# Kernel optimization log

Measured on AMD Instinct MI355X. Metric: run time of the kernel, lower is better.

Reference implementation:

```python
import jax, jax.numpy as jnp
import numpy as np

PROCESS_INIT = 1.0
OBSERVATION_INIT = 1.0


def _build_dynamics_A(K, fut_len):
    # shift-structured single-modal A: state slot i takes value of slot i+1, last step repeats
    sd = 2 * fut_len
    a = np.zeros((sd, sd), dtype=np.float32)
    for i in range(fut_len - 1):
        a[2 * i, 2 * i + 2] = 1.0
        a[2 * i + 1, 2 * i + 3] = 1.0
    a[sd - 2, sd - 2] = 1.0
    a[sd - 1, sd - 1] = 1.0
    # block-diagonal over K modes
    return jnp.asarray(np.kron(np.eye(K, dtype=np.float32), a))


def setup_inputs() -> dict:
    key = jax.random.key(0)
    ks = jax.random.split(key, 6)
    B, A, K, fut_len = 2, 32, 6, 30
    D = K * 2 * fut_len  # 360
    belief_mean = jax.random.normal(ks[0], (B, A, D), dtype=jnp.float32)
    M = jax.random.normal(ks[1], (B, A, D, D), dtype=jnp.float32)
    # symmetric, SPD (eigenvalues ~ 2 +/- 0.2) so linear solves are well-posed
    belief_covariance = 0.003 * (M + jnp.swapaxes(M, -1, -2)) + 2.0 * jnp.eye(D, dtype=jnp.float32)
    observations = jax.random.normal(ks[2], (B, A, D), dtype=jnp.float32)
    rs = jax.random.uniform(ks[3], (B, A), dtype=jnp.float32)
    initialized = jax.random.bernoulli(ks[4], 0.7, (B, A))
    selected = jax.random.bernoulli(ks[5], 0.8, (B, A))
    return {
        "belief_mean": belief_mean,
        "belief_covariance": belief_covariance,
        "observations": observations,
        "rs": rs,
        "initialized": initialized,
        "selected": selected,
        "K": K,
        "fut_len": fut_len,
    }


def reference(belief_mean, belief_covariance, observations, rs, initialized, selected, K, fut_len):
    D = K * 2 * fut_len
    A = _build_dynamics_A(K, fut_len)  # [D, D], static sparse shift structure
    I = jnp.eye(D, dtype=belief_mean.dtype)
    r_obs = (rs + OBSERVATION_INIT)[..., None, None]  # [B, A, 1, 1]

    init_new = selected & (~initialized)  # first observation of agent
    upd = selected & initialized          # predict + Kalman update

    # --- initialization branch ---
    mean_init = observations
    cov_init = belief_covariance + r_obs * I

    # --- predict step: m <- A m ; P <- A P A^T + Q, Q = process_init * I ---
    m_pred = belief_mean @ A.T  # [B, A, D]
    P_pred = jnp.einsum('ij,bnjk,lk->bnil', A, belief_covariance, A) + PROCESS_INIT * I

    # --- update step (H = I): S = P + R ; Kg = P S^{-1} ---
    S = P_pred + r_obs * I
    Kg = P_pred @ jnp.linalg.inv(S)
    m_upd = m_pred + jnp.einsum('bnij,bnj->bni', Kg, observations - m_pred)
    P_upd = (I - Kg) @ P_pred

    # --- scatter the three branches back (masked merge) ---
    mean_out = jnp.where(init_new[..., None], mean_init,
               jnp.where(upd[..., None], m_upd, belief_mean))
    cov_out = jnp.where(init_new[..., None, None], cov_init,
              jnp.where(upd[..., None, None], P_upd, belief_covariance))
    initialized_out = initialized | selected
    return mean_out, cov_out, initialized_out
```

## Files before the change

kernel.cpp:

```cpp
#include <hip/hip_runtime.h>

#define D 360
#define NAG 64
#define NB 60
#define NPAN 6
#define COV_OFF (NAG * D)
#define INIT_OFF (COV_OFF + NAG * D * D)
#define RBOFF(par, ag, ct) ((((par) * NAG + (ag)) * 6 + (ct)) * 3600)

__device__ __forceinline__ int gshift(int i) {
    return ((i % 60) < 58) ? (i + 2) : i;
}

__global__ __launch_bounds__(384) void build_kernel(
    const float* __restrict__ P, const float* __restrict__ mean_in,
    const float* __restrict__ obs, const float* __restrict__ rs,
    const int* __restrict__ init_f, const int* __restrict__ sel_f,
    float* __restrict__ out, float* __restrict__ rb)
{
    const int by = blockIdx.x, ag = blockIdx.y, t = threadIdx.x;
    const bool ini = init_f[ag] != 0, sel = sel_f[ag] != 0;
    const float c = rs[ag] + 1.0f;
    if (by == 45) {
        if (t < D) {
            float v = (sel && !ini) ? obs[ag * D + t] : mean_in[ag * D + t];
            out[ag * D + t] = v;
        }
        if (t == 0) out[INIT_OFF + ag] = (ini || sel) ? 1.0f : 0.0f;
        return;
    }
    if (t >= D) return;
    const float* Pa = P + (size_t)ag * D * D;
    float* cov = out + COV_OFF + (size_t)ag * D * D;
    const int j = t;
    if (sel && ini) {
        const int gj = gshift(j);
        #pragma unroll
        for (int s = 0; s < 8; ++s) {
            const int i = by * 8 + s;
            float v = Pa[(size_t)gshift(i) * D + gj];
            if (i == j) v += 1.0f + c;
            cov[(size_t)i * D + j] = v;
            if (i < NB && j >= NB)
                rb[RBOFF(0, ag, j / NB) + i * NB + (j % NB)] = v;
        }
    } else if (sel) {
        #pragma unroll
        for (int s = 0; s < 8; ++s) {
            const int i = by * 8 + s;
            cov[(size_t)i * D + j] = Pa[(size_t)i * D + j] + ((i == j) ? c : 0.0f);
        }
    } else {
        #pragma unroll
        for (int s = 0; s < 8; ++s) {
            const int i = by * 8 + s;
            cov[(size_t)i * D + j] = Pa[(size_t)i * D + j];
        }
    }
}

__device__ __forceinline__ void inv4(float4& m0, float4& m1, float4& m2, float4& m3)
{
    float pv, f;
    pv = 1.0f / m0.x;
    m0.y *= pv; m0.z *= pv; m0.w *= pv; m0.x = pv;
    f = m1.x; m1.y = fmaf(-f, m0.y, m1.y); m1.z = fmaf(-f, m0.z, m1.z); m1.w = fmaf(-f, m0.w, m1.w); m1.x = -f * pv;
    f = m2.x; m2.y = fmaf(-f, m0.y, m2.y); m2.z = fmaf(-f, m0.z, m2.z); m2.w = fmaf(-f, m0.w, m2.w); m2.x = -f * pv;
    f = m3.x; m3.y = fmaf(-f, m0.y, m3.y); m3.z = fmaf(-f, m0.z, m3.z); m3.w = fmaf(-f, m0.w, m3.w); m3.x = -f * pv;
    pv = 1.0f / m1.y;
    m1.x *= pv; m1.z *= pv; m1.w *= pv; m1.y = pv;
    f = m0.y; m0.x = fmaf(-f, m1.x, m0.x); m0.z = fmaf(-f, m1.z, m0.z); m0.w = fmaf(-f, m1.w, m0.w); m0.y = -f * pv;
    f = m2.y; m2.x = fmaf(-f, m1.x, m2.x); m2.z = fmaf(-f, m1.z, m2.z); m2.w = fmaf(-f, m1.w, m2.w); m2.y = -f * pv;
    f = m3.y; m3.x = fmaf(-f, m1.x, m3.x); m3.z = fmaf(-f, m1.z, m3.z); m3.w = fmaf(-f, m1.w, m3.w); m3.y = -f * pv;
    pv = 1.0f / m2.z;
    m2.x *= pv; m2.y *= pv; m2.w *= pv; m2.z = pv;
    f = m0.z; m0.x = fmaf(-f, m2.x, m0.x); m0.y = fmaf(-f, m2.y, m0.y); m0.w = fmaf(-f, m2.w, m0.w); m0.z = -f * pv;
    f = m1.z; m1.x = fmaf(-f, m2.x, m1.x); m1.y = fmaf(-f, m2.y, m1.y); m1.w = fmaf(-f, m2.w, m1.w); m1.z = -f * pv;
    f = m3.z; m3.x = fmaf(-f, m2.x, m3.x); m3.y = fmaf(-f, m2.y, m3.y); m3.w = fmaf(-f, m2.w, m3.w); m3.z = -f * pv;
    pv = 1.0f / m3.w;
    m3.x *= pv; m3.y *= pv; m3.z *= pv; m3.w = pv;
    f = m0.w; m0.x = fmaf(-f, m3.x, m0.x); m0.y = fmaf(-f, m3.y, m0.y); m0.z = fmaf(-f, m3.z, m0.z); m0.w = -f * pv;
    f = m1.w; m1.x = fmaf(-f, m3.x, m1.x); m1.y = fmaf(-f, m3.y, m1.y); m1.z = fmaf(-f, m3.z, m1.z); m1.w = -f * pv;
    f = m2.w; m2.x = fmaf(-f, m3.x, m2.x); m2.y = fmaf(-f, m3.y, m2.y); m2.z = fmaf(-f, m3.z, m2.z); m2.w = -f * pv;
}

__global__ __launch_bounds__(384) void factor_kernel(
    float* __restrict__ out, const int* __restrict__ init_f,
    const int* __restrict__ sel_f, float* __restrict__ rb, int p)
{
    const int ag = blockIdx.x;
    if (!(init_f[ag] && sel_f[ag])) return;
    float* M = out + COV_OFF + (size_t)ag * D * D;
    const int j0 = p * NB;
    const int r = threadIdx.x;
    const int rel = r - j0;
    float4 row[15];
    if (r < D) {
        const float* src = M + (size_t)r * D + j0;
        #pragma unroll
        for (int q = 0; q < 15; ++q) row[q] = *(const float4*)(src + 4 * q);
    }
    __shared__ float4 praw[2][4][15];
    if (rel >= 0 && rel < 4) {
        #pragma unroll
        for (int q = 0; q < 15; ++q) praw[0][rel][q] = row[q];
    }
    __syncthreads();
    #pragma unroll
    for (int kb = 0; kb < 15; ++kb) {
        const int buf = kb & 1;
        float4 m0 = praw[buf][0][kb];
        float4 m1 = praw[buf][1][kb];
        float4 m2 = praw[buf][2][kb];
        float4 m3 = praw[buf][3][kb];
        inv4(m0, m1, m2, m3);
        if (r < D) {
            const bool is_piv = (rel >= 4 * kb) && (rel < 4 * kb + 4);
            float4 sc;
            if (is_piv) {
                const int i = rel - 4 * kb;
                sc = (i == 0) ? m0 : (i == 1) ? m1 : (i == 2) ? m2 : m3;
                #pragma unroll
                for (int q = 0; q < 15; ++q)
                    if (q != kb) row[q] = make_float4(0.f, 0.f, 0.f, 0.f);
            } else {
                float4 fr = row[kb];
                sc.x = -(fr.x * m0.x + fr.y * m1.x + fr.z * m2.x + fr.w * m3.x);
                sc.y = -(fr.x * m0.y + fr.y * m1.y + fr.z * m2.y + fr.w * m3.y);
                sc.z = -(fr.x * m0.z + fr.y * m1.z + fr.z * m2.z + fr.w * m3.z);
                sc.w = -(fr.x * m0.w + fr.y * m1.w + fr.z * m2.w + fr.w * m3.w);
            }
            #pragma unroll
            for (int q = 0; q < 15; ++q) {
                if (q == kb) continue;
                float4 p0 = praw[buf][0][q];
                float4 p1 = praw[buf][1][q];
                float4 p2 = praw[buf][2][q];
                float4 p3 = praw[buf][3][q];
                row[q].x = fmaf(sc.x, p0.x, fmaf(sc.y, p1.x, fmaf(sc.z, p2.x, fmaf(sc.w, p3.x, row[q].x))));
                row[q].y = fmaf(sc.x, p0.y, fmaf(sc.y, p1.y, fmaf(sc.z, p2.y, fmaf(sc.w, p3.y, row[q].y))));
                row[q].z = fmaf(sc.x, p0.z, fmaf(sc.y, p1.z, fmaf(sc.z, p2.z, fmaf(sc.w, p3.z, row[q].z))));
                row[q].w = fmaf(sc.x, p0.w, fmaf(sc.y, p1.w, fmaf(sc.z, p2.w, fmaf(sc.w, p3.w, row[q].w))));
            }
            row[kb] = sc;
            if (kb < 14 && rel >= 4 * (kb + 1) && rel < 4 * (kb + 1) + 4) {
                const int i = rel - 4 * (kb + 1);
                #pragma unroll
                for (int q = 0; q < 15; ++q) praw[buf ^ 1][i][q] = row[q];
            }
        }
        __syncthreads();
    }
    if (r < D) {
        float* dst = M + (size_t)r * D + j0;
        #pragma unroll
        for (int q = 0; q < 15; ++q) *(float4*)(dst + 4 * q) = row[q];
        if (p < NPAN - 1) {
            const int nrel = r - NB * (p + 1);
            if (nrel >= 0 && nrel < NB) {
                float* rdst = rb + RBOFF((p + 1) & 1, ag, p) + nrel * NB;
                #pragma unroll
                for (int q = 0; q < 15; ++q) *(float4*)(rdst + 4 * q) = row[q];
            }
        }
    }
}

__device__ __forceinline__ void mm_row(const float4 a, const float4 b0, const float4 b1,
                                       const float4 b2, const float4 b3, float acc[4]) {
    acc[0] = fmaf(a.x, b0.x, fmaf(a.y, b1.x, fmaf(a.z, b2.x, fmaf(a.w, b3.x, acc[0]))));
    acc[1] = fmaf(a.x, b0.y, fmaf(a.y, b1.y, fmaf(a.z, b2.y, fmaf(a.w, b3.y, acc[1]))));
    acc[2] = fmaf(a.x, b0.z, fmaf(a.y, b1.z, fmaf(a.z, b2.z, fmaf(a.w, b3.z, acc[2]))));
    acc[3] = fmaf(a.x, b0.w, fmaf(a.y, b1.w, fmaf(a.z, b2.w, fmaf(a.w, b3.w, acc[3]))));
}

__global__ __launch_bounds__(256) void update_kernel(
    float* __restrict__ out, const float* __restrict__ rs,
    const int* __restrict__ init_f, const int* __restrict__ sel_f,
    float* __restrict__ rb, int p)
{
    const int ag = blockIdx.x;
    if (!(init_f[ag] && sel_f[ag])) return;
    const int ct = blockIdx.y + (blockIdx.y >= p ? 1 : 0);
    float* M = out + COV_OFF + (size_t)ag * D * D;
    const int j0 = p * NB, c0 = ct * NB;
    const float c = rs[ag] + 1.0f;
    const float c2 = c * c;
    __shared__ float R[NB][NB + 8];
    __shared__ float F[NB][NB + 8];
    const int t = threadIdx.x;
    {
        const float* rsrc = rb + RBOFF(p & 1, ag, ct);
        for (int idx = t; idx < NB * 15; idx += 256) {
            int k = idx / 15, q = idx % 15;
            *(float4*)&R[k][4 * q] = *(const float4*)(rsrc + k * NB + 4 * q);
        }
    }
    const int tx = t % 16, ty = t / 16;
    for (int rr = 0; rr < 2; ++rr) {
        const int rt = (int)blockIdx.z * 2 + rr;
        const int r0 = rt * NB;
        __syncthreads();
        for (int idx = t; idx < NB * 15; idx += 256) {
            int rrw = idx / 15, q = idx % 15;
            *(float4*)&F[rrw][4 * q] = *(const float4*)(M + (size_t)(r0 + rrw) * D + j0 + 4 * q);
        }
        __syncthreads();
        if (tx < 15 && ty < 15) {
            float acc[4][4];
            #pragma unroll
            for (int i = 0; i < 4; ++i)
                #pragma unroll
                for (int j = 0; j < 4; ++j) acc[i][j] = 0.0f;
            for (int kq = 0; kq < 15; ++kq) {
                float4 a0 = *(const float4*)&F[4 * ty + 0][4 * kq];
                float4 a1 = *(const float4*)&F[4 * ty + 1][4 * kq];
                float4 a2 = *(const float4*)&F[4 * ty + 2][4 * kq];
                float4 a3 = *(const float4*)&F[4 * ty + 3][4 * kq];
                float4 b0 = *(const float4*)&R[4 * kq + 0][4 * tx];
                float4 b1 = *(const float4*)&R[4 * kq + 1][4 * tx];
                float4 b2 = *(const float4*)&R[4 * kq + 2][4 * tx];
                float4 b3 = *(const float4*)&R[4 * kq + 3][4 * tx];
                mm_row(a0, b0, b1, b2, b3, acc[0]);
                mm_row(a1, b0, b1, b2, b3, acc[1]);
                mm_row(a2, b0, b1, b2, b3, acc[2]);
                mm_row(a3, b0, b1, b2, b3, acc[3]);
            }
            #pragma unroll
            for (int i = 0; i < 4; ++i) {
                const int rg = r0 + 4 * ty + i;
                float* dst = M + (size_t)rg * D + c0 + 4 * tx;
                float4 base;
                if (rt == p) { base = make_float4(0.f, 0.f, 0.f, 0.f); }
                else         { base = *(const float4*)dst; }
                float4 v;
                v.x = base.x + acc[i][0];
                v.y = base.y + acc[i][1];
                v.z = base.z + acc[i][2];
                v.w = base.w + acc[i][3];
                if (p < NPAN - 1) {
                    if (rt == p + 1 && ct != p + 1) {
                        float* rdst = rb + RBOFF((p + 1) & 1, ag, ct) + (4 * ty + i) * NB + 4 * tx;
                        *(float4*)rdst = v;
                    }
                    *(float4*)dst = v;
                } else {
                    const int cg = c0 + 4 * tx;
                    float4 o;
                    o.x = ((rg == cg + 0) ? c : 0.f) - c2 * v.x;
                    o.y = ((rg == cg + 1) ? c : 0.f) - c2 * v.y;
                    o.z = ((rg == cg + 2) ? c : 0.f) - c2 * v.z;
                    o.w = ((rg == cg + 3) ? c : 0.f) - c2 * v.w;
                    *(float4*)dst = o;
                }
            }
        }
    }
}

__global__ __launch_bounds__(384) void fin_panel_kernel(
    float* __restrict__ out, const float* __restrict__ rs,
    const int* __restrict__ init_f, const int* __restrict__ sel_f)
{
    const int ag = blockIdx.x;
    if (!(init_f[ag] && sel_f[ag])) return;
    const int t = threadIdx.x;
    if (t >= 360) return;
    const float c = rs[ag] + 1.0f;
    const float c2 = c * c;
    float* cov = out + COV_OFF + (size_t)ag * D * D;
    const int r = (int)blockIdx.y * 6 + t / 60;
    const int cc = (NPAN - 1) * NB + (t % 60);
    const float v = cov[(size_t)r * D + cc];
    cov[(size_t)r * D + cc] = ((r == cc) ? c : 0.f) - c2 * v;
}

__global__ __launch_bounds__(384) void solve_mean_kernel(
    float* __restrict__ out, const float* __restrict__ mean_in,
    const float* __restrict__ obs, const float* __restrict__ rs,
    const int* __restrict__ init_f, const int* __restrict__ sel_f)
{
    const int ag = blockIdx.x;
    if (!(init_f[ag] && sel_f[ag])) return;
    const float* C = out + COV_OFF + (size_t)ag * D * D;
    __shared__ float dsh[D];
    const int t = threadIdx.x;
    if (t < D) dsh[t] = obs[ag * D + t] - mean_in[ag * D + gshift(t)];
    __syncthreads();
    if (t < D) {
        float dot = 0.0f;
        #pragma unroll 8
        for (int j = 0; j < D; ++j)
            dot = fmaf(C[(size_t)j * D + t], dsh[j], dot);
        const float c = rs[ag] + 1.0f;
        out[ag * D + t] = obs[ag * D + t] - dsh[t] + dot / c;
    }
}

extern "C" void kernel_launch(void* const* d_in, const int* in_sizes, int n_in,
                              void* d_out, int out_size, void* d_ws, size_t ws_size,
                              hipStream_t stream) {
    const float* mean_in     = (const float*)d_in[0];
    const float* P           = (const float*)d_in[1];
    const float* obs         = (const float*)d_in[2];
    const float* rs          = (const float*)d_in[3];
    const int*   initialized = (const int*)d_in[4];
    const int*   selected    = (const int*)d_in[5];
    float* out = (float*)d_out;
    float* rb  = (float*)d_ws;

    build_kernel<<<dim3(46, NAG), 384, 0, stream>>>(P, mean_in, obs, rs,
                                                    initialized, selected, out, rb);
    for (int p = 0; p < NPAN; ++p) {
        factor_kernel<<<NAG, 384, 0, stream>>>(out, initialized, selected, rb, p);
        update_kernel<<<dim3(NAG, NPAN - 1, 3), 256, 0, stream>>>(out, rs, initialized,
                                                                  selected, rb, p);
    }
    fin_panel_kernel<<<dim3(NAG, 60), 384, 0, stream>>>(out, rs, initialized, selected);
    solve_mean_kernel<<<NAG, 384, 0, stream>>>(out, mean_in, obs, rs, initialized, selected);
}
```

Measured before the change: 312.9 us.

## Widen Gauss-Jordan panels to 120 columns and fold final panel scaling

Raises the block Gauss-Jordan inversion panel width from 60 to 120, so the factor/update loop runs 3 times instead of 6. That halves the kernel launches and the global round trips of the trailing matrix. The update kernel now handles 60x60 output tiles with a 120-deep inner product, and the factor kernel applies the final (c - c^2*X) transform for the last panel, which removes the separate fin_panel kernel. In exchange each factor thread holds 30 float4 registers and runs 30 serial 4x4 pivot steps, which may hurt occupancy and lengthen the serial factor phase.

```diff
diff --git a/kernel.cpp b/kernel.cpp
--- a/kernel.cpp
+++ b/kernel.cpp
@@ -2,11 +2,12 @@
 
 #define D 360
 #define NAG 64
-#define NB 60
-#define NPAN 6
+#define NB 120
+#define NPAN 3
+#define NQ 30
 #define COV_OFF (NAG * D)
 #define INIT_OFF (COV_OFF + NAG * D * D)
-#define RBOFF(par, ag, ct) ((((par) * NAG + (ag)) * 6 + (ct)) * 3600)
+#define SB(par, ag, slot) ((((size_t)(par) * NAG + (ag)) * 4 + (slot)) * 7200)
 
 __device__ __forceinline__ int gshift(int i) {
     return ((i % 60) < 58) ? (i + 2) : i;
@@ -42,7 +43,7 @@
             if (i == j) v += 1.0f + c;
             cov[(size_t)i * D + j] = v;
             if (i < NB && j >= NB)
-                rb[RBOFF(0, ag, j / NB) + i * NB + (j % NB)] = v;
+                rb[SB(0, ag, j / 60 - 2) + i * 60 + (j % 60)] = v;
         }
     } else if (sel) {
         #pragma unroll
@@ -84,9 +85,69 @@
     f = m2.w; m2.x = fmaf(-f, m3.x, m2.x); m2.y = fmaf(-f, m3.y, m2.y); m2.z = fmaf(-f, m3.z, m2.z); m2.w = -f * pv;
 }
 
+template<int KB>
+__device__ __forceinline__ void gj_step(float4 (&row)[NQ], int r, int rel,
+                                        float4 (&praw)[2][4][NQ])
+{
+    const int buf = KB & 1;
+    float4 m0 = praw[buf][0][KB];
+    float4 m1 = praw[buf][1][KB];
+    float4 m2 = praw[buf][2][KB];
+    float4 m3 = praw[buf][3][KB];
+    inv4(m0, m1, m2, m3);
+    if (r < D) {
+        const bool is_piv = (rel >= 4 * KB) && (rel < 4 * KB + 4);
+        float4 sc;
+        if (is_piv) {
+            const int i = rel - 4 * KB;
+            sc = (i == 0) ? m0 : (i == 1) ? m1 : (i == 2) ? m2 : m3;
+            #pragma unroll
+            for (int q = 0; q < NQ; ++q)
+                if (q != KB) row[q] = make_float4(0.f, 0.f, 0.f, 0.f);
+        } else {
+            float4 fr = row[KB];
+            sc.x = -(fr.x * m0.x + fr.y * m1.x + fr.z * m2.x + fr.w * m3.x);
+            sc.y = -(fr.x * m0.y + fr.y * m1.y + fr.z * m2.y + fr.w * m3.y);
+            sc.z = -(fr.x * m0.z + fr.y * m1.z + fr.z * m2.z + fr.w * m3.z);
+            sc.w = -(fr.x * m0.w + fr.y * m1.w + fr.z * m2.w + fr.w * m3.w);
+        }
+        #pragma unroll
+        for (int q = 0; q < NQ; ++q) {
+            if (q == KB) continue;
+            float4 p0 = praw[buf][0][q];
+            float4 p1 = praw[buf][1][q];
+            float4 p2 = praw[buf][2][q];
+            float4 p3 = praw[buf][3][q];
+            row[q].x = fmaf(sc.x, p0.x, fmaf(sc.y, p1.x, fmaf(sc.z, p2.x, fmaf(sc.w, p3.x, row[q].x))));
+            row[q].y = fmaf(sc.x, p0.y, fmaf(sc.y, p1.y, fmaf(sc.z, p2.y, fmaf(sc.w, p3.y, row[q].y))));
+            row[q].z = fmaf(sc.x, p0.z, fmaf(sc.y, p1.z, fmaf(sc.z, p2.z, fmaf(sc.w, p3.z, row[q].z))));
+            row[q].w = fmaf(sc.x, p0.w, fmaf(sc.y, p1.w, fmaf(sc.z, p2.w, fmaf(sc.w, p3.w, row[q].w))));
+        }
+        row[KB] = sc;
+        if (KB < NQ - 1 && rel >= 4 * (KB + 1) && rel < 4 * (KB + 1) + 4) {
+            const int i = rel - 4 * (KB + 1);
+            #pragma unroll
+            for (int q = 0; q < NQ; ++q) praw[buf ^ 1][i][q] = row[q];
+        }
+    }
+    __syncthreads();
+}
+
+template<int KB> struct GJSteps {
+    __device__ static __forceinline__ void run(float4 (&row)[NQ], int r, int rel,
+                                               float4 (&praw)[2][4][NQ]) {
+        gj_step<KB>(row, r, rel, praw);
+        GJSteps<KB + 1>::run(row, r, rel, praw);
+    }
+};
+template<> struct GJSteps<NQ> {
+    __device__ static __forceinline__ void run(float4 (&)[NQ], int, int, float4 (&)[2][4][NQ]) {}
+};
+
 __global__ __launch_bounds__(384) void factor_kernel(
-    float* __restrict__ out, const int* __restrict__ init_f,
-    const int* __restrict__ sel_f, float* __restrict__ rb, int p)
+    float* __restrict__ out, const float* __restrict__ rs,
+    const int* __restrict__ init_f, const int* __restrict__ sel_f,
+    float* __restrict__ rb, int p)
 {
     const int ag = blockIdx.x;
     if (!(init_f[ag] && sel_f[ag])) return;
@@ -94,73 +155,45 @@
     const int j0 = p * NB;
     const int r = threadIdx.x;
     const int rel = r - j0;
-    float4 row[15];
+    float4 row[NQ];
     if (r < D) {
         const float* src = M + (size_t)r * D + j0;
         #pragma unroll
-        for (int q = 0; q < 15; ++q) row[q] = *(const float4*)(src + 4 * q);
-    }
-    __shared__ float4 praw[2][4][15];
+        for (int q = 0; q < NQ; ++q) row[q] = *(const float4*)(src + 4 * q);
+    }
+    __shared__ float4 praw[2][4][NQ];
     if (rel >= 0 && rel < 4) {
         #pragma unroll
-        for (int q = 0; q < 15; ++q) praw[0][rel][q] = row[q];
+        for (int q = 0; q < NQ; ++q) praw[0][rel][q] = row[q];
     }
     __syncthreads();
-    #pragma unroll
-    for (int kb = 0; kb < 15; ++kb) {
-        const int buf = kb & 1;
-        float4 m0 = praw[buf][0][kb];
-        float4 m1 = praw[buf][1][kb];
-        float4 m2 = praw[buf][2][kb];
-        float4 m3 = praw[buf][3][kb];
-        inv4(m0, m1, m2, m3);
-        if (r < D) {
-            const bool is_piv = (rel >= 4 * kb) && (rel < 4 * kb + 4);
-            float4 sc;
-            if (is_piv) {
-                const int i = rel - 4 * kb;
-                sc = (i == 0) ? m0 : (i == 1) ? m1 : (i == 2) ? m2 : m3;
-                #pragma unroll
-                for (int q = 0; q < 15; ++q)
-                    if (q != kb) row[q] = make_float4(0.f, 0.f, 0.f, 0.f);
-            } else {
-                float4 fr = row[kb];
-                sc.x = -(fr.x * m0.x + fr.y * m1.x + fr.z * m2.x + fr.w * m3.x);
-                sc.y = -(fr.x * m0.y + fr.y * m1.y + fr.z * m2.y + fr.w * m3.y);
-                sc.z = -(fr.x * m0.z + fr.y * m1.z + fr.z * m2.z + fr.w * m3.z);
-                sc.w = -(fr.x * m0.w + fr.y * m1.w + fr.z * m2.w + fr.w * m3.w);
-            }
-            #pragma unroll
-            for (int q = 0; q < 15; ++q) {
-                if (q == kb) continue;
-                float4 p0 = praw[buf][0][q];
-                float4 p1 = praw[buf][1][q];
-                float4 p2 = praw[buf][2][q];
-                float4 p3 = praw[buf][3][q];
-                row[q].x = fmaf(sc.x, p0.x, fmaf(sc.y, p1.x, fmaf(sc.z, p2.x, fmaf(sc.w, p3.x, row[q].x))));
-                row[q].y = fmaf(sc.x, p0.y, fmaf(sc.y, p1.y, fmaf(sc.z, p2.y, fmaf(sc.w, p3.y, row[q].y))));
-                row[q].z = fmaf(sc.x, p0.z, fmaf(sc.y, p1.z, fmaf(sc.z, p2.z, fmaf(sc.w, p3.z, row[q].z))));
-                row[q].w = fmaf(sc.x, p0.w, fmaf(sc.y, p1.w, fmaf(sc.z, p2.w, fmaf(sc.w, p3.w, row[q].w))));
-            }
-            row[kb] = sc;
-            if (kb < 14 && rel >= 4 * (kb + 1) && rel < 4 * (kb + 1) + 4) {
-                const int i = rel - 4 * (kb + 1);
-                #pragma unroll
-                for (int q = 0; q < 15; ++q) praw[buf ^ 1][i][q] = row[q];
-            }
-        }
-        __syncthreads();
-    }
+    GJSteps<0>::run(row, r, rel, praw);
     if (r < D) {
         float* dst = M + (size_t)r * D + j0;
-        #pragma unroll
-        for (int q = 0; q < 15; ++q) *(float4*)(dst + 4 * q) = row[q];
-        if (p < NPAN - 1) {
+        if (p == NPAN - 1) {
+            const float c = rs[ag] + 1.0f;
+            const float c2 = c * c;
+            #pragma unroll
+            for (int q = 0; q < NQ; ++q) {
+                const int cg = j0 + 4 * q;
+                float4 o;
+                o.x = ((r == cg + 0) ? c : 0.f) - c2 * row[q].x;
+                o.y = ((r == cg + 1) ? c : 0.f) - c2 * row[q].y;
+                o.z = ((r == cg + 2) ? c : 0.f) - c2 * row[q].z;
+                o.w = ((r == cg + 3) ? c : 0.f) - c2 * row[q].w;
+                *(float4*)(dst + 4 * q) = o;
+            }
+        } else {
+            #pragma unroll
+            for (int q = 0; q < NQ; ++q) *(float4*)(dst + 4 * q) = row[q];
             const int nrel = r - NB * (p + 1);
             if (nrel >= 0 && nrel < NB) {
-                float* rdst = rb + RBOFF((p + 1) & 1, ag, p) + nrel * NB;
                 #pragma unroll
-                for (int q = 0; q < 15; ++q) *(float4*)(rdst + 4 * q) = row[q];
+                for (int q = 0; q < NQ; ++q) {
+                    const int slot = 2 * p + (q >= 15);
+                    float* rdst = rb + SB((p + 1) & 1, ag, slot) + nrel * 60 + (q % 15) * 4;
+                    *(float4*)rdst = row[q];
+                }
             }
         }
     }
@@ -181,98 +214,90 @@
 {
     const int ag = blockIdx.x;
     if (!(init_f[ag] && sel_f[ag])) return;
-    const int ct = blockIdx.y + (blockIdx.y >= p ? 1 : 0);
+    const int y = blockIdx.y;
+    const int ct = y + (y >= 2 * p ? 2 : 0);
+    const int rt = blockIdx.z;
+    const int r0 = 60 * rt, c0 = 60 * ct;
+    const bool panelrow = ((rt >> 1) == p);
     float* M = out + COV_OFF + (size_t)ag * D * D;
-    const int j0 = p * NB, c0 = ct * NB;
     const float c = rs[ag] + 1.0f;
     const float c2 = c * c;
-    __shared__ float R[NB][NB + 8];
-    __shared__ float F[NB][NB + 8];
+    __shared__ float R[NB][60];
+    __shared__ float F[60][NB + 4];
     const int t = threadIdx.x;
     {
-        const float* rsrc = rb + RBOFF(p & 1, ag, ct);
-        for (int idx = t; idx < NB * 15; idx += 256) {
-            int k = idx / 15, q = idx % 15;
-            *(float4*)&R[k][4 * q] = *(const float4*)(rsrc + k * NB + 4 * q);
-        }
-    }
+        const float* rsrc = rb + SB(p & 1, ag, y);
+        for (int idx = t; idx < 120 * 15; idx += 256) {
+            const int k = idx / 15, q = idx % 15;
+            *(float4*)&R[k][4 * q] = *(const float4*)(rsrc + k * 60 + 4 * q);
+        }
+    }
+    {
+        for (int idx = t; idx < 60 * NQ; idx += 256) {
+            const int row = idx / NQ, q = idx % NQ;
+            float4 v = *(const float4*)(M + (size_t)(r0 + row) * D + p * NB + 4 * q);
+            if (p == NPAN - 1) {
+                const int rg = r0 + row, cg = p * NB + 4 * q;
+                v.x = (((rg == cg + 0) ? c : 0.f) - v.x) / c2;
+                v.y = (((rg == cg + 1) ? c : 0.f) - v.y) / c2;
+                v.z = (((rg == cg + 2) ? c : 0.f) - v.z) / c2;
+                v.w = (((rg == cg + 3) ? c : 0.f) - v.w) / c2;
+            }
+            *(float4*)&F[row][4 * q] = v;
+        }
+    }
+    __syncthreads();
     const int tx = t % 16, ty = t / 16;
-    for (int rr = 0; rr < 2; ++rr) {
-        const int rt = (int)blockIdx.z * 2 + rr;
-        const int r0 = rt * NB;
-        __syncthreads();
-        for (int idx = t; idx < NB * 15; idx += 256) {
-            int rrw = idx / 15, q = idx % 15;
-            *(float4*)&F[rrw][4 * q] = *(const float4*)(M + (size_t)(r0 + rrw) * D + j0 + 4 * q);
-        }
-        __syncthreads();
-        if (tx < 15 && ty < 15) {
-            float acc[4][4];
-            #pragma unroll
-            for (int i = 0; i < 4; ++i)
-                #pragma unroll
-                for (int j = 0; j < 4; ++j) acc[i][j] = 0.0f;
-            for (int kq = 0; kq < 15; ++kq) {
-                float4 a0 = *(const float4*)&F[4 * ty + 0][4 * kq];
-                float4 a1 = *(const float4*)&F[4 * ty + 1][4 * kq];
-                float4 a2 = *(const float4*)&F[4 * ty + 2][4 * kq];
-                float4 a3 = *(const float4*)&F[4 * ty + 3][4 * kq];
-                float4 b0 = *(const float4*)&R[4 * kq + 0][4 * tx];
-                float4 b1 = *(const float4*)&R[4 * kq + 1][4 * tx];
-                float4 b2 = *(const float4*)&R[4 * kq + 2][4 * tx];
-                float4 b3 = *(const float4*)&R[4 * kq + 3][4 * tx];
-                mm_row(a0, b0, b1, b2, b3, acc[0]);
-                mm_row(a1, b0, b1, b2, b3, acc[1]);
-                mm_row(a2, b0, b1, b2, b3, acc[2]);
-                mm_row(a3, b0, b1, b2, b3, acc[3]);
+    if (tx < 15 && ty < 15) {
+        float acc[4][4];
+        #pragma unroll
+        for (int i = 0; i < 4; ++i)
+            #pragma unroll
+            for (int j = 0; j < 4; ++j) acc[i][j] = 0.0f;
+        for (int kq = 0; kq < NQ; ++kq) {
+            float4 a0 = *(const float4*)&F[4 * ty + 0][4 * kq];
+            float4 a1 = *(const float4*)&F[4 * ty + 1][4 * kq];
+            float4 a2 = *(const float4*)&F[4 * ty + 2][4 * kq];
+            float4 a3 = *(const float4*)&F[4 * ty + 3][4 * kq];
+            float4 b0 = *(const float4*)&R[4 * kq + 0][4 * tx];
+            float4 b1 = *(const float4*)&R[4 * kq + 1][4 * tx];
+            float4 b2 = *(const float4*)&R[4 * kq + 2][4 * tx];
+            float4 b3 = *(const float4*)&R[4 * kq + 3][4 * tx];
+            mm_row(a0, b0, b1, b2, b3, acc[0]);
+            mm_row(a1, b0, b1, b2, b3, acc[1]);
+            mm_row(a2, b0, b1, b2, b3, acc[2]);
+            mm_row(a3, b0, b1, b2, b3, acc[3]);
+        }
+        #pragma unroll
+        for (int i = 0; i < 4; ++i) {
+            const int rg = r0 + 4 * ty + i;
+            float* dst = M + (size_t)rg * D + c0 + 4 * tx;
+            float4 base;
+            if (panelrow) { base = make_float4(0.f, 0.f, 0.f, 0.f); }
+            else          { base = *(const float4*)dst; }
+            float4 v;
+            v.x = base.x + acc[i][0];
+            v.y = base.y + acc[i][1];
+            v.z = base.z + acc[i][2];
+            v.w = base.w + acc[i][3];
+            if (p < NPAN - 1) {
+                if ((rt >> 1) == p + 1 && (ct >> 1) != p + 1) {
+                    const int slot = ct - (ct > 2 * p + 3 ? 2 : 0);
+                    const int srow = rg - NB * (p + 1);
+                    *(float4*)(rb + SB((p + 1) & 1, ag, slot) + srow * 60 + 4 * tx) = v;
+                }
+                *(float4*)dst = v;
+            } else {
+                const int cg = c0 + 4 * tx;
+                float4 o;
+                o.x = ((rg == cg + 0) ? c : 0.f) - c2 * v.x;
+                o.y = ((rg == cg + 1) ? c : 0.f) - c2 * v.y;
+                o.z = ((rg == cg + 2) ? c : 0.f) - c2 * v.z;
+                o.w = ((rg == cg + 3) ? c : 0.f) - c2 * v.w;
+                *(float4*)dst = o;
             }
-            #pragma unroll
-            for (int i = 0; i < 4; ++i) {
-                const int rg = r0 + 4 * ty + i;
-                float* dst = M + (size_t)rg * D + c0 + 4 * tx;
-                float4 base;
-                if (rt == p) { base = make_float4(0.f, 0.f, 0.f, 0.f); }
-                else         { base = *(const float4*)dst; }
-                float4 v;
-                v.x = base.x + acc[i][0];
-                v.y = base.y + acc[i][1];
-                v.z = base.z + acc[i][2];
-                v.w = base.w + acc[i][3];
-                if (p < NPAN - 1) {
-                    if (rt == p + 1 && ct != p + 1) {
-                        float* rdst = rb + RBOFF((p + 1) & 1, ag, ct) + (4 * ty + i) * NB + 4 * tx;
-                        *(float4*)rdst = v;
-                    }
-                    *(float4*)dst = v;
-                } else {
-                    const int cg = c0 + 4 * tx;
-                    float4 o;
-                    o.x = ((rg == cg + 0) ? c : 0.f) - c2 * v.x;
-                    o.y = ((rg == cg + 1) ? c : 0.f) - c2 * v.y;
-                    o.z = ((rg == cg + 2) ? c : 0.f) - c2 * v.z;
-                    o.w = ((rg == cg + 3) ? c : 0.f) - c2 * v.w;
-                    *(float4*)dst = o;
-                }
-            }
-        }
-    }
-}
-
-__global__ __launch_bounds__(384) void fin_panel_kernel(
-    float* __restrict__ out, const float* __restrict__ rs,
-    const int* __restrict__ init_f, const int* __restrict__ sel_f)
-{
-    const int ag = blockIdx.x;
-    if (!(init_f[ag] && sel_f[ag])) return;
-    const int t = threadIdx.x;
-    if (t >= 360) return;
-    const float c = rs[ag] + 1.0f;
-    const float c2 = c * c;
-    float* cov = out + COV_OFF + (size_t)ag * D * D;
-    const int r = (int)blockIdx.y * 6 + t / 60;
-    const int cc = (NPAN - 1) * NB + (t % 60);
-    const float v = cov[(size_t)r * D + cc];
-    cov[(size_t)r * D + cc] = ((r == cc) ? c : 0.f) - c2 * v;
+        }
+    }
 }
 
 __global__ __launch_bounds__(384) void solve_mean_kernel(
@@ -312,10 +337,9 @@
     build_kernel<<<dim3(46, NAG), 384, 0, stream>>>(P, mean_in, obs, rs,
                                                     initialized, selected, out, rb);
     for (int p = 0; p < NPAN; ++p) {
-        factor_kernel<<<NAG, 384, 0, stream>>>(out, initialized, selected, rb, p);
-        update_kernel<<<dim3(NAG, NPAN - 1, 3), 256, 0, stream>>>(out, rs, initialized,
-                                                                  selected, rb, p);
-    }
-    fin_panel_kernel<<<dim3(NAG, 60), 384, 0, stream>>>(out, rs, initialized, selected);
+        factor_kernel<<<NAG, 384, 0, stream>>>(out, rs, initialized, selected, rb, p);
+        update_kernel<<<dim3(NAG, 4, 6), 256, 0, stream>>>(out, rs, initialized,
+                                                           selected, rb, p);
+    }
     solve_mean_kernel<<<NAG, 384, 0, stream>>>(out, mean_in, obs, rs, initialized, selected);
 }
```

New measurement: 366.1 us. +17.0%, slower.

## Stage factor panel in shared memory with 540 threads; fold final panel transform

Applied to the files above, without the earlier changes.

The panel factorization now keeps the 360x60 slab in shared memory and spreads it over 540 threads, each handling one float4 column chunk for ten rows. Before, each of 360 threads held a full 60-wide row in registers. The aim is more parallelism per block and lower register pressure in the serial per-panel step. The final-panel output transform is now applied inside factor_kernel for the last panel, and update_kernel undoes it when reading that panel. This removes the separate fin_panel_kernel launch, at the cost of extra LDS traffic and a divide in the update loads.

```diff
diff --git a/kernel.cpp b/kernel.cpp
--- a/kernel.cpp
+++ b/kernel.cpp
@@ -4,6 +4,7 @@
 #define NAG 64
 #define NB 60
 #define NPAN 6
+#define FTH 540
 #define COV_OFF (NAG * D)
 #define INIT_OFF (COV_OFF + NAG * D * D)
 #define RBOFF(par, ag, ct) ((((par) * NAG + (ag)) * 6 + (ct)) * 3600)
@@ -84,84 +85,96 @@
     f = m2.w; m2.x = fmaf(-f, m3.x, m2.x); m2.y = fmaf(-f, m3.y, m2.y); m2.z = fmaf(-f, m3.z, m2.z); m2.w = -f * pv;
 }
 
-__global__ __launch_bounds__(384) void factor_kernel(
-    float* __restrict__ out, const int* __restrict__ init_f,
-    const int* __restrict__ sel_f, float* __restrict__ rb, int p)
+__global__ __launch_bounds__(FTH) void factor_kernel(
+    float* __restrict__ out, const float* __restrict__ rs,
+    const int* __restrict__ init_f, const int* __restrict__ sel_f,
+    float* __restrict__ rb, int p)
 {
     const int ag = blockIdx.x;
     if (!(init_f[ag] && sel_f[ag])) return;
     float* M = out + COV_OFF + (size_t)ag * D * D;
     const int j0 = p * NB;
-    const int r = threadIdx.x;
-    const int rel = r - j0;
-    float4 row[15];
-    if (r < D) {
-        const float* src = M + (size_t)r * D + j0;
-        #pragma unroll
-        for (int q = 0; q < 15; ++q) row[q] = *(const float4*)(src + 4 * q);
-    }
+    const int t = threadIdx.x;
+    __shared__ float  slab[D][NB];
     __shared__ float4 praw[2][4][15];
-    if (rel >= 0 && rel < 4) {
-        #pragma unroll
-        for (int q = 0; q < 15; ++q) praw[0][rel][q] = row[q];
+    __shared__ float4 fcol[2][D];
+    const int q  = t % 15;
+    const int r0 = t / 15;
+    #pragma unroll
+    for (int k = 0; k < 10; ++k) {
+        const int r = r0 + 36 * k;
+        *(float4*)&slab[r][4 * q] = *(const float4*)(M + (size_t)r * D + j0 + 4 * q);
     }
     __syncthreads();
-    #pragma unroll
+    if (t < 60) praw[0][t / 15][t % 15] = *(float4*)&slab[j0 + t / 15][4 * (t % 15)];
+    if (t < D)  fcol[0][t] = *(float4*)&slab[t][0];
+    __syncthreads();
+
     for (int kb = 0; kb < 15; ++kb) {
         const int buf = kb & 1;
-        float4 m0 = praw[buf][0][kb];
-        float4 m1 = praw[buf][1][kb];
-        float4 m2 = praw[buf][2][kb];
-        float4 m3 = praw[buf][3][kb];
+        float4 m0 = praw[buf][0][kb], m1 = praw[buf][1][kb],
+               m2 = praw[buf][2][kb], m3 = praw[buf][3][kb];
         inv4(m0, m1, m2, m3);
-        if (r < D) {
-            const bool is_piv = (rel >= 4 * kb) && (rel < 4 * kb + 4);
+        const int pr0 = j0 + 4 * kb;
+        #pragma unroll
+        for (int k = 0; k < 10; ++k) {
+            const int r = r0 + 36 * k;
+            const int ii = r - pr0;
+            const bool ispiv = (ii >= 0) && (ii < 4);
             float4 sc;
-            if (is_piv) {
-                const int i = rel - 4 * kb;
-                sc = (i == 0) ? m0 : (i == 1) ? m1 : (i == 2) ? m2 : m3;
-                #pragma unroll
-                for (int q = 0; q < 15; ++q)
-                    if (q != kb) row[q] = make_float4(0.f, 0.f, 0.f, 0.f);
+            if (ispiv) {
+                sc = (ii == 0) ? m0 : (ii == 1) ? m1 : (ii == 2) ? m2 : m3;
             } else {
-                float4 fr = row[kb];
+                const float4 fr = fcol[buf][r];
                 sc.x = -(fr.x * m0.x + fr.y * m1.x + fr.z * m2.x + fr.w * m3.x);
                 sc.y = -(fr.x * m0.y + fr.y * m1.y + fr.z * m2.y + fr.w * m3.y);
                 sc.z = -(fr.x * m0.z + fr.y * m1.z + fr.z * m2.z + fr.w * m3.z);
                 sc.w = -(fr.x * m0.w + fr.y * m1.w + fr.z * m2.w + fr.w * m3.w);
             }
-            #pragma unroll
-            for (int q = 0; q < 15; ++q) {
-                if (q == kb) continue;
-                float4 p0 = praw[buf][0][q];
-                float4 p1 = praw[buf][1][q];
-                float4 p2 = praw[buf][2][q];
-                float4 p3 = praw[buf][3][q];
-                row[q].x = fmaf(sc.x, p0.x, fmaf(sc.y, p1.x, fmaf(sc.z, p2.x, fmaf(sc.w, p3.x, row[q].x))));
-                row[q].y = fmaf(sc.x, p0.y, fmaf(sc.y, p1.y, fmaf(sc.z, p2.y, fmaf(sc.w, p3.y, row[q].y))));
-                row[q].z = fmaf(sc.x, p0.z, fmaf(sc.y, p1.z, fmaf(sc.z, p2.z, fmaf(sc.w, p3.z, row[q].z))));
-                row[q].w = fmaf(sc.x, p0.w, fmaf(sc.y, p1.w, fmaf(sc.z, p2.w, fmaf(sc.w, p3.w, row[q].w))));
-            }
-            row[kb] = sc;
-            if (kb < 14 && rel >= 4 * (kb + 1) && rel < 4 * (kb + 1) + 4) {
-                const int i = rel - 4 * (kb + 1);
-                #pragma unroll
-                for (int q = 0; q < 15; ++q) praw[buf ^ 1][i][q] = row[q];
+            float4 v;
+            if (q == kb) {
+                v = sc;
+            } else {
+                const float4 p0 = praw[buf][0][q], p1 = praw[buf][1][q],
+                             p2 = praw[buf][2][q], p3 = praw[buf][3][q];
+                float4 b;
+                if (ispiv) b = make_float4(0.f, 0.f, 0.f, 0.f);
+                else       b = *(float4*)&slab[r][4 * q];
+                v.x = fmaf(sc.x, p0.x, fmaf(sc.y, p1.x, fmaf(sc.z, p2.x, fmaf(sc.w, p3.x, b.x))));
+                v.y = fmaf(sc.x, p0.y, fmaf(sc.y, p1.y, fmaf(sc.z, p2.y, fmaf(sc.w, p3.y, b.y))));
+                v.z = fmaf(sc.x, p0.z, fmaf(sc.y, p1.z, fmaf(sc.z, p2.z, fmaf(sc.w, p3.z, b.z))));
+                v.w = fmaf(sc.x, p0.w, fmaf(sc.y, p1.w, fmaf(sc.z, p2.w, fmaf(sc.w, p3.w, b.w))));
+            }
+            *(float4*)&slab[r][4 * q] = v;
+            if (kb < 14) {
+                if (q == kb + 1) fcol[buf ^ 1][r] = v;
+                const int ni = r - (pr0 + 4);
+                if (ni >= 0 && ni < 4) praw[buf ^ 1][ni][q] = v;
             }
         }
         __syncthreads();
     }
-    if (r < D) {
-        float* dst = M + (size_t)r * D + j0;
-        #pragma unroll
-        for (int q = 0; q < 15; ++q) *(float4*)(dst + 4 * q) = row[q];
-        if (p < NPAN - 1) {
+
+    const float c = rs[ag] + 1.0f;
+    const float c2 = c * c;
+    #pragma unroll
+    for (int k = 0; k < 10; ++k) {
+        const int r = r0 + 36 * k;
+        const float4 v = *(float4*)&slab[r][4 * q];
+        float* dst = M + (size_t)r * D + j0 + 4 * q;
+        if (p == NPAN - 1) {
+            const int cg = j0 + 4 * q;
+            float4 o;
+            o.x = ((r == cg + 0) ? c : 0.f) - c2 * v.x;
+            o.y = ((r == cg + 1) ? c : 0.f) - c2 * v.y;
+            o.z = ((r == cg + 2) ? c : 0.f) - c2 * v.z;
+            o.w = ((r == cg + 3) ? c : 0.f) - c2 * v.w;
+            *(float4*)dst = o;
+        } else {
+            *(float4*)dst = v;
             const int nrel = r - NB * (p + 1);
-            if (nrel >= 0 && nrel < NB) {
-                float* rdst = rb + RBOFF((p + 1) & 1, ag, p) + nrel * NB;
-                #pragma unroll
-                for (int q = 0; q < 15; ++q) *(float4*)(rdst + 4 * q) = row[q];
-            }
+            if (nrel >= 0 && nrel < NB)
+                *(float4*)(rb + RBOFF((p + 1) & 1, ag, p) + nrel * NB + 4 * q) = v;
         }
     }
 }
@@ -192,8 +205,8 @@
     {
         const float* rsrc = rb + RBOFF(p & 1, ag, ct);
         for (int idx = t; idx < NB * 15; idx += 256) {
-            int k = idx / 15, q = idx % 15;
-            *(float4*)&R[k][4 * q] = *(const float4*)(rsrc + k * NB + 4 * q);
+            int k = idx / 15, qq = idx % 15;
+            *(float4*)&R[k][4 * qq] = *(const float4*)(rsrc + k * NB + 4 * qq);
         }
     }
     const int tx = t % 16, ty = t / 16;
@@ -202,8 +215,16 @@
         const int r0 = rt * NB;
         __syncthreads();
         for (int idx = t; idx < NB * 15; idx += 256) {
-            int rrw = idx / 15, q = idx % 15;
-            *(float4*)&F[rrw][4 * q] = *(const float4*)(M + (size_t)(r0 + rrw) * D + j0 + 4 * q);
+            int rrw = idx / 15, qq = idx % 15;
+            float4 v = *(const float4*)(M + (size_t)(r0 + rrw) * D + j0 + 4 * qq);
+            if (p == NPAN - 1) {
+                const int rg = r0 + rrw, cg = j0 + 4 * qq;
+                v.x = (((rg == cg + 0) ? c : 0.f) - v.x) / c2;
+                v.y = (((rg == cg + 1) ? c : 0.f) - v.y) / c2;
+                v.z = (((rg == cg + 2) ? c : 0.f) - v.z) / c2;
+                v.w = (((rg == cg + 3) ? c : 0.f) - v.w) / c2;
+            }
+            *(float4*)&F[rrw][4 * qq] = v;
         }
         __syncthreads();
         if (tx < 15 && ty < 15) {
@@ -258,23 +279,6 @@
     }
 }
 
-__global__ __launch_bounds__(384) void fin_panel_kernel(
-    float* __restrict__ out, const float* __restrict__ rs,
-    const int* __restrict__ init_f, const int* __restrict__ sel_f)
-{
-    const int ag = blockIdx.x;
-    if (!(init_f[ag] && sel_f[ag])) return;
-    const int t = threadIdx.x;
-    if (t >= 360) return;
-    const float c = rs[ag] + 1.0f;
-    const float c2 = c * c;
-    float* cov = out + COV_OFF + (size_t)ag * D * D;
-    const int r = (int)blockIdx.y * 6 + t / 60;
-    const int cc = (NPAN - 1) * NB + (t % 60);
-    const float v = cov[(size_t)r * D + cc];
-    cov[(size_t)r * D + cc] = ((r == cc) ? c : 0.f) - c2 * v;
-}
-
 __global__ __launch_bounds__(384) void solve_mean_kernel(
     float* __restrict__ out, const float* __restrict__ mean_in,
     const float* __restrict__ obs, const float* __restrict__ rs,
@@ -312,10 +316,9 @@
     build_kernel<<<dim3(46, NAG), 384, 0, stream>>>(P, mean_in, obs, rs,
                                                     initialized, selected, out, rb);
     for (int p = 0; p < NPAN; ++p) {
-        factor_kernel<<<NAG, 384, 0, stream>>>(out, initialized, selected, rb, p);
+        factor_kernel<<<NAG, FTH, 0, stream>>>(out, rs, initialized, selected, rb, p);
         update_kernel<<<dim3(NAG, NPAN - 1, 3), 256, 0, stream>>>(out, rs, initialized,
                                                                   selected, rb, p);
     }
-    fin_panel_kernel<<<dim3(NAG, 60), 384, 0, stream>>>(out, rs, initialized, selected);
     solve_mean_kernel<<<NAG, 384, 0, stream>>>(out, mean_in, obs, rs, initialized, selected);
 }
```

Result: slower. 539.1 us (+72.3%).
